# Kernel tuning notes

Hardware: AMD Instinct MI355X
Metric: run time of the kernel (lower is better)

## Reference

```python
import jax, jax.numpy as jnp
import numpy as np

D_MODEL = 1024
D_FF = 4096
N_EXPERTS = 8
TOP_K = 2
AUX_COEF = 0.01
ZLOSS_COEF = 0.001
EPS = 1e-9


def setup_inputs() -> dict:
    key = jax.random.key(0)
    k0, k1, k2, k3 = jax.random.split(key, 4)
    x = jax.random.normal(k0, (4, 2048, D_MODEL), dtype=jnp.float32)
    router_w = jax.random.normal(k1, (N_EXPERTS, D_MODEL), dtype=jnp.float32) * 0.02
    w1 = jax.random.normal(k2, (N_EXPERTS, D_FF, D_MODEL), dtype=jnp.float32) * 0.02
    b1 = jnp.zeros((N_EXPERTS, D_FF), dtype=jnp.float32)
    w2 = jax.random.normal(k3, (N_EXPERTS, D_MODEL, D_FF), dtype=jnp.float32) * 0.02
    b2 = jnp.zeros((N_EXPERTS, D_MODEL), dtype=jnp.float32)
    return {"x": x, "router_w": router_w, "w1": w1, "b1": b1, "w2": w2, "b2": b2}


def reference(x, router_w, w1, b1, w2, b2):
    B, T, D = x.shape
    N = B * T
    xf = x.reshape(N, D)

    # Router: logits [N, E], softmax probs, top-k selection + renormalized weights
    logits = jnp.einsum('nd,ed->ne', xf, router_w)
    probs = jax.nn.softmax(logits, axis=-1)
    topk_vals, topk_idx = jax.lax.top_k(probs, TOP_K)  # [N, K]
    topk_w = topk_vals / (topk_vals.sum(axis=-1, keepdims=True) + EPS)

    # Dense combine weights [N, E] (top-k indices are unique per row)
    combine = jnp.zeros((N, N_EXPERTS), dtype=xf.dtype)
    combine = combine.at[jnp.arange(N)[:, None], topk_idx].add(topk_w)

    # Per-expert MLP (fixed small loop over experts), weighted combine.
    # drop_tokens=False => no capacity truncation; masked-dense == gather/scatter math.
    y = jnp.zeros_like(xf)
    for e in range(N_EXPERTS):
        h = jax.nn.gelu(jnp.einsum('nd,fd->nf', xf, w1[e]) + b1[e], approximate=False)
        out_e = jnp.einsum('nf,df->nd', h, w2[e]) + b2[e]
        y = y + out_e * combine[:, e:e + 1]

    # Aux losses / stats
    importance = probs.sum(axis=0)                                   # [E]
    expert_load = jnp.zeros((N_EXPERTS,), jnp.float32).at[topk_idx.reshape(-1)].add(1.0)
    imp_n = importance / (importance.sum() + EPS)
    load_n = expert_load / (expert_load.sum() + EPS)
    balance_loss = N_EXPERTS * jnp.sum(imp_n * load_n)
    z_loss = jnp.mean(jax.nn.logsumexp(logits, axis=-1) ** 2)
    aux_loss = AUX_COEF * balance_loss + ZLOSS_COEF * z_loss

    return y.reshape(B, T, D), aux_loss, expert_load, importance
```

## Files before the change

### kernel.cpp

```cpp
#include <hip/hip_runtime.h>
#include <math.h>

#define NTOK 8192
#define DMODEL 1024
#define DFF 4096
#define NEXP 8
#define TILE 128
#define MAXTILES 136
#define MAXROWS (MAXTILES * TILE)
#define MOE_EPS 1e-9f
#define REG64 8192

typedef unsigned short u16;
typedef __bf16 bf16x8 __attribute__((ext_vector_type(8)));
typedef float f32x4 __attribute__((ext_vector_type(4)));

struct Ctrl {
    int counts[NEXP];
    int fill[NEXP];
    int padded_off[NEXP];
    int n_tiles;
    int tile_expert[MAXTILES];
    int tile_base[MAXTILES];
    int tile_valid[MAXTILES];
    float imp[NEXP];
    float zacc;
};

__device__ __forceinline__ u16 f2bf(float f) {
    unsigned u = __float_as_uint(f);
    unsigned r = u + 0x7fffu + ((u >> 16) & 1u);
    return (u16)(r >> 16);
}

__device__ __forceinline__ void load16(const void* g, void* l) {
    __builtin_amdgcn_global_load_lds((__attribute__((address_space(1))) void*)g,
                                     (__attribute__((address_space(3))) void*)l,
                                     16, 0, 0);
}

__device__ __forceinline__ float gelu_fast(float h) {
    float u = h * (1.5957691216f + 0.0713548162f * h * h);
    return h / (1.f + __expf(-u));
}

__global__ __launch_bounds__(256) void k_convert(const float* __restrict__ src,
                                                 u16* __restrict__ dst, int n4) {
    int i = blockIdx.x * 256 + threadIdx.x;
    int stride = gridDim.x * 256;
    for (; i < n4; i += stride) {
        float4 v = ((const float4*)src)[i];
        ushort4 o;
        o.x = f2bf(v.x); o.y = f2bf(v.y); o.z = f2bf(v.z); o.w = f2bf(v.w);
        ((ushort4*)dst)[i] = o;
    }
}

__global__ __launch_bounds__(256) void k_router(const float* __restrict__ x,
                                                const float* __restrict__ rw,
                                                u16* __restrict__ xb,
                                                int* __restrict__ top_idx,
                                                float* __restrict__ top_w,
                                                Ctrl* __restrict__ ctrl) {
    __shared__ float srw[NEXP * DMODEL];
    __shared__ float simp[NEXP];
    __shared__ float szl;
    int tid = threadIdx.x;
    for (int i = tid; i < NEXP * DMODEL / 4; i += 256)
        ((float4*)srw)[i] = ((const float4*)rw)[i];
    if (tid < NEXP) simp[tid] = 0.f;
    if (tid == 0) szl = 0.f;
    __syncthreads();

    int lane = tid & 63;
    int n = blockIdx.x * 4 + (tid >> 6);
    float p[NEXP];
#pragma unroll
    for (int e = 0; e < NEXP; ++e) p[e] = 0.f;
    const float4* xr = (const float4*)(x + (size_t)n * DMODEL);
    u16 xs[16];
#pragma unroll
    for (int j = 0; j < 4; ++j) {
        float4 xv = xr[lane * 4 + j];
        int d = (lane * 4 + j) * 4;
        xs[j * 4 + 0] = f2bf(xv.x);
        xs[j * 4 + 1] = f2bf(xv.y);
        xs[j * 4 + 2] = f2bf(xv.z);
        xs[j * 4 + 3] = f2bf(xv.w);
#pragma unroll
        for (int e = 0; e < NEXP; ++e) {
            const float* r = srw + e * DMODEL + d;
            p[e] += xv.x * r[0] + xv.y * r[1] + xv.z * r[2] + xv.w * r[3];
        }
    }
    {
        uint4* dst = (uint4*)(xb + (size_t)n * DMODEL + lane * 16);
        dst[0] = ((const uint4*)xs)[0];
        dst[1] = ((const uint4*)xs)[1];
    }
#pragma unroll
    for (int e = 0; e < NEXP; ++e) {
#pragma unroll
        for (int off = 32; off > 0; off >>= 1) p[e] += __shfl_xor(p[e], off);
    }
    if (lane == 0) {
        float m = p[0];
#pragma unroll
        for (int e = 1; e < NEXP; ++e) m = fmaxf(m, p[e]);
        float pr[NEXP];
        float s = 0.f;
#pragma unroll
        for (int e = 0; e < NEXP; ++e) { pr[e] = expf(p[e] - m); s += pr[e]; }
        float inv = 1.f / s;
#pragma unroll
        for (int e = 0; e < NEXP; ++e) pr[e] *= inv;
        float lse = m + logf(s);
        int i0 = 0; float v0 = pr[0];
#pragma unroll
        for (int e = 1; e < NEXP; ++e) if (pr[e] > v0) { v0 = pr[e]; i0 = e; }
        int i1 = -1; float v1 = -1.f;
#pragma unroll
        for (int e = 0; e < NEXP; ++e) if (e != i0 && pr[e] > v1) { v1 = pr[e]; i1 = e; }
        float den = v0 + v1 + MOE_EPS;
        top_idx[n * 2] = i0;
        top_idx[n * 2 + 1] = i1;
        top_w[n * 2] = v0 / den;
        top_w[n * 2 + 1] = v1 / den;
#pragma unroll
        for (int e = 0; e < NEXP; ++e) atomicAdd(&simp[e], pr[e]);
        atomicAdd(&szl, lse * lse);
    }
    __syncthreads();
    if (tid < NEXP) atomicAdd(&ctrl->imp[tid], simp[tid]);
    if (tid == 255) atomicAdd(&ctrl->zacc, szl);
}

__global__ __launch_bounds__(256) void k_build(const int* __restrict__ top_idx,
                                               Ctrl* __restrict__ ctrl,
                                               int* __restrict__ tok_idx,
                                               float* __restrict__ tok_w) {
    __shared__ int cnt[NEXP];
    __shared__ int off[NEXP];
    __shared__ int tiles[NEXP];
    int tid = threadIdx.x;
    if (tid < NEXP) cnt[tid] = 0;
    __syncthreads();
    for (int i = tid; i < NTOK * 2; i += 256) atomicAdd(&cnt[top_idx[i]], 1);
    __syncthreads();
    if (tid == 0) {
        int o = 0, t = 0;
        for (int e = 0; e < NEXP; ++e) {
            int c = cnt[e];
            int te = (c + TILE - 1) / TILE;
            ctrl->counts[e] = c;
            ctrl->padded_off[e] = o;
            off[e] = o;
            tiles[e] = te;
            for (int i = 0; i < te; ++i) {
                ctrl->tile_expert[t] = e;
                ctrl->tile_base[t] = o + i * TILE;
                int v = c - i * TILE;
                ctrl->tile_valid[t] = v > TILE ? TILE : v;
                ++t;
            }
            o += te * TILE;
        }
        ctrl->n_tiles = t;
    }
    __syncthreads();
    for (int e = 0; e < NEXP; ++e) {
        int start = off[e] + cnt[e];
        int end = off[e] + tiles[e] * TILE;
        for (int i = start + tid; i < end; i += 256) {
            tok_idx[i] = 0;
            tok_w[i] = 0.f;
        }
    }
}

__global__ __launch_bounds__(256) void k_fill(const int* __restrict__ top_idx,
                                              const float* __restrict__ top_w,
                                              Ctrl* __restrict__ ctrl,
                                              int* __restrict__ tok_idx,
                                              float* __restrict__ tok_w) {
    int n = blockIdx.x * 256 + threadIdx.x;
    if (n >= NTOK) return;
#pragma unroll
    for (int k = 0; k < 2; ++k) {
        int e = top_idx[n * 2 + k];
        int pos = atomicAdd(&ctrl->fill[e], 1);
        int slot = ctrl->padded_off[e] + pos;
        tok_idx[slot] = n;
        tok_w[slot] = top_w[n * 2 + k];
    }
}

#define KLOOPM97(STA, STB, NK)                                                        \
    for (int kt = 0; kt < (NK); ++kt) {                                               \
        STA(kt); STB(kt);                                                             \
        asm volatile("s_waitcnt vmcnt(0)" ::: "memory");                              \
        __builtin_amdgcn_s_barrier();                                                 \
        bf16x8 a[4], b[4];                                                            \
        _Pragma("unroll") for (int m = 0; m < 4; ++m) a[m] = *(const bf16x8*)(sA + aoff[m] + csw0); \
        _Pragma("unroll") for (int n = 0; n < 4; ++n) b[n] = *(const bf16x8*)(sB + boff[n] + csw0); \
        __builtin_amdgcn_s_setprio(1);                                                \
        _Pragma("unroll") for (int m = 0; m < 4; ++m)                                 \
            _Pragma("unroll") for (int n = 0; n < 4; ++n)                             \
                acc[m][n] = __builtin_amdgcn_mfma_f32_16x16x32_bf16(a[m], b[n], acc[m][n], 0, 0, 0); \
        __builtin_amdgcn_s_setprio(0);                                                \
        _Pragma("unroll") for (int m = 0; m < 4; ++m) a[m] = *(const bf16x8*)(sA + aoff[m] + csw1); \
        _Pragma("unroll") for (int n = 0; n < 4; ++n) b[n] = *(const bf16x8*)(sB + boff[n] + csw1); \
        __builtin_amdgcn_s_setprio(1);                                                \
        _Pragma("unroll") for (int m = 0; m < 4; ++m)                                 \
            _Pragma("unroll") for (int n = 0; n < 4; ++n)                             \
                acc[m][n] = __builtin_amdgcn_mfma_f32_16x16x32_bf16(a[m], b[n], acc[m][n], 0, 0, 0); \
        __builtin_amdgcn_s_setprio(0);                                                \
        __builtin_amdgcn_s_barrier();                                                 \
    }

__global__ __launch_bounds__(256, 4) void k_gemm1(const u16* __restrict__ xb,
                                                  const u16* __restrict__ w1b,
                                                  const float* __restrict__ b1,
                                                  const int* __restrict__ tok_idx,
                                                  const Ctrl* __restrict__ ctrl,
                                                  u16* __restrict__ H) {
    int flat = blockIdx.x;
    int t = (flat & 7) + ((flat >> 8) << 3);
    int n0 = ((flat >> 3) & 31) * TILE;
    if (t >= ctrl->n_tiles) return;
    int e = ctrl->tile_expert[t];
    int rbase = ctrl->tile_base[t];

    __shared__ __align__(16) u16 sA[REG64];
    __shared__ __align__(16) u16 sB[REG64];

    int tid = threadIdx.x;
    const u16* aS[4];
    const u16* bS[4];
    int fo[4];
#pragma unroll
    for (int q = 0; q < 4; ++q) {
        int f = q * 256 + tid;
        int row = f >> 3;
        int lc = (f & 7) ^ (row & 7);
        aS[q] = xb + (size_t)tok_idx[rbase + row] * DMODEL + lc * 8;
        bS[q] = w1b + (size_t)e * DFF * DMODEL + (size_t)(n0 + row) * DMODEL + lc * 8;
        fo[q] = f * 8;
    }

#define STA1(kt)                                                                      \
    do { _Pragma("unroll") for (int q = 0; q < 4; ++q)                                \
        load16(aS[q] + (kt) * 64, &sA[fo[q]]); } while (0)
#define STB1(kt)                                                                      \
    do { _Pragma("unroll") for (int q = 0; q < 4; ++q)                                \
        load16(bS[q] + (kt) * 64, &sB[fo[q]]); } while (0)

    int lane = tid & 63, w = tid >> 6;
    int wr = w >> 1, wc = w & 1;
    int l15 = lane & 15, lg = lane >> 4;
    int bank7 = l15 & 7;
    int csw0 = ((lg + 0) ^ bank7) * 8;
    int csw1 = ((lg + 4) ^ bank7) * 8;

    int aoff[4], boff[4];
#pragma unroll
    for (int m = 0; m < 4; ++m) aoff[m] = (wr * 64 + m * 16 + l15) * 64;
#pragma unroll
    for (int n = 0; n < 4; ++n) boff[n] = (wc * 64 + n * 16 + l15) * 64;

    f32x4 acc[4][4];
#pragma unroll
    for (int m = 0; m < 4; ++m)
#pragma unroll
        for (int n = 0; n < 4; ++n) acc[m][n] = (f32x4){0.f, 0.f, 0.f, 0.f};

    KLOOPM97(STA1, STB1, DMODEL / 64)
#undef STA1
#undef STB1

    float bias[4];
#pragma unroll
    for (int n = 0; n < 4; ++n) bias[n] = b1[e * DFF + n0 + wc * 64 + n * 16 + l15];
#pragma unroll
    for (int m = 0; m < 4; ++m)
#pragma unroll
        for (int n = 0; n < 4; ++n) {
            int gcol = n0 + wc * 64 + n * 16 + l15;
#pragma unroll
            for (int r = 0; r < 4; ++r) {
                int grow = wr * 64 + m * 16 + lg * 4 + r;
                float h = acc[m][n][r] + bias[n];
                H[(size_t)(rbase + grow) * DFF + gcol] = f2bf(gelu_fast(h));
            }
        }
}

__global__ __launch_bounds__(256, 4) void k_gemm2(const u16* __restrict__ H,
                                                  const u16* __restrict__ w2b,
                                                  const float* __restrict__ b2,
                                                  const int* __restrict__ tok_idx,
                                                  const float* __restrict__ tok_w,
                                                  const Ctrl* __restrict__ ctrl,
                                                  float* __restrict__ y) {
    int flat = blockIdx.x;
    int t = (flat & 7) + ((flat >> 6) << 3);
    int n0 = ((flat >> 3) & 7) * TILE;
    if (t >= ctrl->n_tiles) return;
    int e = ctrl->tile_expert[t];
    int rbase = ctrl->tile_base[t];
    int valid = ctrl->tile_valid[t];

    __shared__ __align__(16) u16 sA[REG64];
    __shared__ __align__(16) u16 sB[REG64];

    int tid = threadIdx.x;
    const u16* aS[4];
    const u16* bS[4];
    int fo[4];
#pragma unroll
    for (int q = 0; q < 4; ++q) {
        int f = q * 256 + tid;
        int row = f >> 3;
        int lc = (f & 7) ^ (row & 7);
        aS[q] = H + (size_t)(rbase + row) * DFF + lc * 8;
        bS[q] = w2b + (size_t)e * DMODEL * DFF + (size_t)(n0 + row) * DFF + lc * 8;
        fo[q] = f * 8;
    }

#define STA2(kt)                                                                      \
    do { _Pragma("unroll") for (int q = 0; q < 4; ++q)                                \
        load16(aS[q] + (kt) * 64, &sA[fo[q]]); } while (0)
#define STB2(kt)                                                                      \
    do { _Pragma("unroll") for (int q = 0; q < 4; ++q)                                \
        load16(bS[q] + (kt) * 64, &sB[fo[q]]); } while (0)

    int lane = tid & 63, w = tid >> 6;
    int wr = w >> 1, wc = w & 1;
    int l15 = lane & 15, lg = lane >> 4;
    int bank7 = l15 & 7;
    int csw0 = ((lg + 0) ^ bank7) * 8;
    int csw1 = ((lg + 4) ^ bank7) * 8;

    int aoff[4], boff[4];
#pragma unroll
    for (int m = 0; m < 4; ++m) aoff[m] = (wr * 64 + m * 16 + l15) * 64;
#pragma unroll
    for (int n = 0; n < 4; ++n) boff[n] = (wc * 64 + n * 16 + l15) * 64;

    f32x4 acc[4][4];
#pragma unroll
    for (int m = 0; m < 4; ++m)
#pragma unroll
        for (int n = 0; n < 4; ++n) acc[m][n] = (f32x4){0.f, 0.f, 0.f, 0.f};

    KLOOPM97(STA2, STB2, DFF / 64)
#undef STA2
#undef STB2

    float bias[4];
#pragma unroll
    for (int n = 0; n < 4; ++n) bias[n] = b2[e * DMODEL + n0 + wc * 64 + n * 16 + l15];
#pragma unroll
    for (int m = 0; m < 4; ++m)
#pragma unroll
        for (int n = 0; n < 4; ++n) {
            int gcol = n0 + wc * 64 + n * 16 + l15;
#pragma unroll
            for (int r = 0; r < 4; ++r) {
                int grow = wr * 64 + m * 16 + lg * 4 + r;
                if (grow < valid) {
                    int slot = rbase + grow;
                    int tok = tok_idx[slot];
                    float wgt = tok_w[slot];
                    unsafeAtomicAdd(&y[(size_t)tok * DMODEL + gcol],
                                    wgt * (acc[m][n][r] + bias[n]));
                }
            }
        }
}

__global__ void k_final(const Ctrl* __restrict__ ctrl, float* __restrict__ out) {
    if (blockIdx.x == 0 && threadIdx.x == 0) {
        float imp[NEXP], ld[NEXP];
        float imps = 0.f, loads = 0.f;
        for (int e = 0; e < NEXP; ++e) {
            imp[e] = ctrl->imp[e];
            ld[e] = (float)ctrl->counts[e];
            imps += imp[e];
            loads += ld[e];
        }
        float bal = 0.f;
        for (int e = 0; e < NEXP; ++e)
            bal += (imp[e] / (imps + MOE_EPS)) * (ld[e] / (loads + MOE_EPS));
        bal *= (float)NEXP;
        float z = ctrl->zacc / (float)NTOK;
        float aux = 0.01f * bal + 0.001f * z;
        size_t base = (size_t)NTOK * DMODEL;
        out[base] = aux;
        for (int e = 0; e < NEXP; ++e) out[base + 1 + e] = ld[e];
        for (int e = 0; e < NEXP; ++e) out[base + 9 + e] = imp[e];
    }
}

extern "C" void kernel_launch(void* const* d_in, const int* in_sizes, int n_in,
                              void* d_out, int out_size, void* d_ws, size_t ws_size,
                              hipStream_t stream) {
    (void)in_sizes; (void)n_in; (void)out_size; (void)ws_size;
    const float* x  = (const float*)d_in[0];
    const float* rw = (const float*)d_in[1];
    const float* w1 = (const float*)d_in[2];
    const float* b1 = (const float*)d_in[3];
    const float* w2 = (const float*)d_in[4];
    const float* b2 = (const float*)d_in[5];
    float* out = (float*)d_out;

    char* p = (char*)d_ws;
    Ctrl* ctrl = (Ctrl*)p;          p += 4096;
    u16* xb    = (u16*)p;           p += (size_t)NTOK * DMODEL * 2;
    u16* w1b   = (u16*)p;           p += (size_t)NEXP * DFF * DMODEL * 2;
    u16* w2b   = (u16*)p;           p += (size_t)NEXP * DMODEL * DFF * 2;
    u16* Hbuf  = (u16*)p;           p += (size_t)MAXROWS * DFF * 2;
    int* tok_idx = (int*)p;         p += (size_t)MAXROWS * 4;
    float* tok_w = (float*)p;       p += (size_t)MAXROWS * 4;
    int* tIdx  = (int*)p;           p += (size_t)NTOK * 2 * 4;
    float* tW  = (float*)p;         p += (size_t)NTOK * 2 * 4;

    hipMemsetAsync(ctrl, 0, sizeof(Ctrl), stream);
    hipMemsetAsync(d_out, 0, (size_t)NTOK * DMODEL * sizeof(float), stream);

    k_convert<<<2048, 256, 0, stream>>>(w1, w1b, NEXP * DFF * DMODEL / 4);
    k_convert<<<2048, 256, 0, stream>>>(w2, w2b, NEXP * DMODEL * DFF / 4);

    k_router<<<NTOK / 4, 256, 0, stream>>>(x, rw, xb, tIdx, tW, ctrl);
    k_build<<<1, 256, 0, stream>>>(tIdx, ctrl, tok_idx, tok_w);
    k_fill<<<NTOK / 256, 256, 0, stream>>>(tIdx, tW, ctrl, tok_idx, tok_w);

    k_gemm1<<<MAXTILES * (DFF / TILE), 256, 0, stream>>>(xb, w1b, b1, tok_idx, ctrl, Hbuf);
    k_gemm2<<<MAXTILES * (DMODEL / TILE), 256, 0, stream>>>(Hbuf, w2b, b2, tok_idx, tok_w, ctrl, out);

    k_final<<<1, 64, 0, stream>>>(ctrl, out);
}
```

Measured before the change: 694.5 us.

## Use persistent grids for expert GEMMs and merge small launches

Both expert GEMM kernels become persistent: a fixed grid of 1024 blocks strides over the tile work list, so blocks no longer launch only to exit on padded tiles. The two weight-conversion launches are merged into one kernel, and the aux-loss finalisation moves into k_build, which removes the k_final launch. The aim is lower launch and early-exit block overhead. The cost is a static striding over work, which can balance load worse than the hardware block scheduler, plus an extra barrier per tile.

After: 738.9 us. 6.4% more time.

```diff
diff --git a/kernel.cpp b/kernel.cpp
--- a/kernel.cpp
+++ b/kernel.cpp
@@ -10,6 +10,7 @@
 #define MAXROWS (MAXTILES * TILE)
 #define MOE_EPS 1e-9f
 #define REG64 8192
+#define PGRID 1024
 
 typedef unsigned short u16;
 typedef __bf16 bf16x8 __attribute__((ext_vector_type(8)));
@@ -44,15 +45,19 @@
     return h / (1.f + __expf(-u));
 }
 
-__global__ __launch_bounds__(256) void k_convert(const float* __restrict__ src,
-                                                 u16* __restrict__ dst, int n4) {
+__global__ __launch_bounds__(256) void k_convert2(const float* __restrict__ s1,
+                                                  u16* __restrict__ d1, int n4a,
+                                                  const float* __restrict__ s2,
+                                                  u16* __restrict__ d2, int n4tot) {
     int i = blockIdx.x * 256 + threadIdx.x;
     int stride = gridDim.x * 256;
-    for (; i < n4; i += stride) {
-        float4 v = ((const float4*)src)[i];
+    for (; i < n4tot; i += stride) {
+        const float4* src = (i < n4a) ? (const float4*)s1 + i : (const float4*)s2 + (i - n4a);
+        ushort4* dst = (i < n4a) ? (ushort4*)d1 + i : (ushort4*)d2 + (i - n4a);
+        float4 v = *src;
         ushort4 o;
         o.x = f2bf(v.x); o.y = f2bf(v.y); o.z = f2bf(v.z); o.w = f2bf(v.w);
-        ((ushort4*)dst)[i] = o;
+        *dst = o;
     }
 }
 
@@ -138,7 +143,8 @@
 __global__ __launch_bounds__(256) void k_build(const int* __restrict__ top_idx,
                                                Ctrl* __restrict__ ctrl,
                                                int* __restrict__ tok_idx,
-                                               float* __restrict__ tok_w) {
+                                               float* __restrict__ tok_w,
+                                               float* __restrict__ out) {
     __shared__ int cnt[NEXP];
     __shared__ int off[NEXP];
     __shared__ int tiles[NEXP];
@@ -166,6 +172,24 @@
             o += te * TILE;
         }
         ctrl->n_tiles = t;
+        float imp[NEXP], ld[NEXP];
+        float imps = 0.f, loads = 0.f;
+        for (int e = 0; e < NEXP; ++e) {
+            imp[e] = ctrl->imp[e];
+            ld[e] = (float)cnt[e];
+            imps += imp[e];
+            loads += ld[e];
+        }
+        float bal = 0.f;
+        for (int e = 0; e < NEXP; ++e)
+            bal += (imp[e] / (imps + MOE_EPS)) * (ld[e] / (loads + MOE_EPS));
+        bal *= (float)NEXP;
+        float z = ctrl->zacc / (float)NTOK;
+        float aux = 0.01f * bal + 0.001f * z;
+        size_t base = (size_t)NTOK * DMODEL;
+        out[base] = aux;
+        for (int e = 0; e < NEXP; ++e) out[base + 1 + e] = ld[e];
+        for (int e = 0; e < NEXP; ++e) out[base + 9 + e] = imp[e];
     }
     __syncthreads();
     for (int e = 0; e < NEXP; ++e) {
@@ -224,29 +248,43 @@
                                                   const int* __restrict__ tok_idx,
                                                   const Ctrl* __restrict__ ctrl,
                                                   u16* __restrict__ H) {
-    int flat = blockIdx.x;
-    int t = (flat & 7) + ((flat >> 8) << 3);
-    int n0 = ((flat >> 3) & 31) * TILE;
-    if (t >= ctrl->n_tiles) return;
-    int e = ctrl->tile_expert[t];
-    int rbase = ctrl->tile_base[t];
-
     __shared__ __align__(16) u16 sA[REG64];
     __shared__ __align__(16) u16 sB[REG64];
 
     int tid = threadIdx.x;
-    const u16* aS[4];
-    const u16* bS[4];
-    int fo[4];
-#pragma unroll
-    for (int q = 0; q < 4; ++q) {
-        int f = q * 256 + tid;
-        int row = f >> 3;
-        int lc = (f & 7) ^ (row & 7);
-        aS[q] = xb + (size_t)tok_idx[rbase + row] * DMODEL + lc * 8;
-        bS[q] = w1b + (size_t)e * DFF * DMODEL + (size_t)(n0 + row) * DMODEL + lc * 8;
-        fo[q] = f * 8;
-    }
+    int lane = tid & 63, w = tid >> 6;
+    int wr = w >> 1, wc = w & 1;
+    int l15 = lane & 15, lg = lane >> 4;
+    int bank7 = l15 & 7;
+    int csw0 = ((lg + 0) ^ bank7) * 8;
+    int csw1 = ((lg + 4) ^ bank7) * 8;
+
+    int aoff[4], boff[4];
+#pragma unroll
+    for (int m = 0; m < 4; ++m) aoff[m] = (wr * 64 + m * 16 + l15) * 64;
+#pragma unroll
+    for (int n = 0; n < 4; ++n) boff[n] = (wc * 64 + n * 16 + l15) * 64;
+
+    int n_tiles = ctrl->n_tiles;
+    for (int wk = blockIdx.x; wk < MAXTILES * 32; wk += PGRID) {
+        int t = (wk & 7) + ((wk >> 8) << 3);
+        int n0 = ((wk >> 3) & 31) * TILE;
+        if (t >= n_tiles) continue;
+        int e = ctrl->tile_expert[t];
+        int rbase = ctrl->tile_base[t];
+
+        const u16* aS[4];
+        const u16* bS[4];
+        int fo[4];
+#pragma unroll
+        for (int q = 0; q < 4; ++q) {
+            int f = q * 256 + tid;
+            int row = f >> 3;
+            int lc = (f & 7) ^ (row & 7);
+            aS[q] = xb + (size_t)tok_idx[rbase + row] * DMODEL + lc * 8;
+            bS[q] = w1b + (size_t)e * DFF * DMODEL + (size_t)(n0 + row) * DMODEL + lc * 8;
+            fo[q] = f * 8;
+        }
 
 #define STA1(kt)                                                                      \
     do { _Pragma("unroll") for (int q = 0; q < 4; ++q)                                \
@@ -255,44 +293,33 @@
     do { _Pragma("unroll") for (int q = 0; q < 4; ++q)                                \
         load16(bS[q] + (kt) * 64, &sB[fo[q]]); } while (0)
 
-    int lane = tid & 63, w = tid >> 6;
-    int wr = w >> 1, wc = w & 1;
-    int l15 = lane & 15, lg = lane >> 4;
-    int bank7 = l15 & 7;
-    int csw0 = ((lg + 0) ^ bank7) * 8;
-    int csw1 = ((lg + 4) ^ bank7) * 8;
-
-    int aoff[4], boff[4];
-#pragma unroll
-    for (int m = 0; m < 4; ++m) aoff[m] = (wr * 64 + m * 16 + l15) * 64;
-#pragma unroll
-    for (int n = 0; n < 4; ++n) boff[n] = (wc * 64 + n * 16 + l15) * 64;
-
-    f32x4 acc[4][4];
-#pragma unroll
-    for (int m = 0; m < 4; ++m)
-#pragma unroll
-        for (int n = 0; n < 4; ++n) acc[m][n] = (f32x4){0.f, 0.f, 0.f, 0.f};
-
-    KLOOPM97(STA1, STB1, DMODEL / 64)
+        f32x4 acc[4][4];
+#pragma unroll
+        for (int m = 0; m < 4; ++m)
+#pragma unroll
+            for (int n = 0; n < 4; ++n) acc[m][n] = (f32x4){0.f, 0.f, 0.f, 0.f};
+
+        KLOOPM97(STA1, STB1, DMODEL / 64)
 #undef STA1
 #undef STB1
 
-    float bias[4];
-#pragma unroll
-    for (int n = 0; n < 4; ++n) bias[n] = b1[e * DFF + n0 + wc * 64 + n * 16 + l15];
-#pragma unroll
-    for (int m = 0; m < 4; ++m)
-#pragma unroll
-        for (int n = 0; n < 4; ++n) {
-            int gcol = n0 + wc * 64 + n * 16 + l15;
-#pragma unroll
-            for (int r = 0; r < 4; ++r) {
-                int grow = wr * 64 + m * 16 + lg * 4 + r;
-                float h = acc[m][n][r] + bias[n];
-                H[(size_t)(rbase + grow) * DFF + gcol] = f2bf(gelu_fast(h));
+        float bias[4];
+#pragma unroll
+        for (int n = 0; n < 4; ++n) bias[n] = b1[e * DFF + n0 + wc * 64 + n * 16 + l15];
+#pragma unroll
+        for (int m = 0; m < 4; ++m)
+#pragma unroll
+            for (int n = 0; n < 4; ++n) {
+                int gcol = n0 + wc * 64 + n * 16 + l15;
+#pragma unroll
+                for (int r = 0; r < 4; ++r) {
+                    int grow = wr * 64 + m * 16 + lg * 4 + r;
+                    float h = acc[m][n][r] + bias[n];
+                    H[(size_t)(rbase + grow) * DFF + gcol] = f2bf(gelu_fast(h));
+                }
             }
-        }
+        __builtin_amdgcn_s_barrier();
+    }
 }
 
 __global__ __launch_bounds__(256, 4) void k_gemm2(const u16* __restrict__ H,
@@ -302,30 +329,44 @@
                                                   const float* __restrict__ tok_w,
                                                   const Ctrl* __restrict__ ctrl,
                                                   float* __restrict__ y) {
-    int flat = blockIdx.x;
-    int t = (flat & 7) + ((flat >> 6) << 3);
-    int n0 = ((flat >> 3) & 7) * TILE;
-    if (t >= ctrl->n_tiles) return;
-    int e = ctrl->tile_expert[t];
-    int rbase = ctrl->tile_base[t];
-    int valid = ctrl->tile_valid[t];
-
     __shared__ __align__(16) u16 sA[REG64];
     __shared__ __align__(16) u16 sB[REG64];
 
     int tid = threadIdx.x;
-    const u16* aS[4];
-    const u16* bS[4];
-    int fo[4];
-#pragma unroll
-    for (int q = 0; q < 4; ++q) {
-        int f = q * 256 + tid;
-        int row = f >> 3;
-        int lc = (f & 7) ^ (row & 7);
-        aS[q] = H + (size_t)(rbase + row) * DFF + lc * 8;
-        bS[q] = w2b + (size_t)e * DMODEL * DFF + (size_t)(n0 + row) * DFF + lc * 8;
-        fo[q] = f * 8;
-    }
+    int lane = tid & 63, w = tid >> 6;
+    int wr = w >> 1, wc = w & 1;
+    int l15 = lane & 15, lg = lane >> 4;
+    int bank7 = l15 & 7;
+    int csw0 = ((lg + 0) ^ bank7) * 8;
+    int csw1 = ((lg + 4) ^ bank7) * 8;
+
+    int aoff[4], boff[4];
+#pragma unroll
+    for (int m = 0; m < 4; ++m) aoff[m] = (wr * 64 + m * 16 + l15) * 64;
+#pragma unroll
+    for (int n = 0; n < 4; ++n) boff[n] = (wc * 64 + n * 16 + l15) * 64;
+
+    int n_tiles = ctrl->n_tiles;
+    for (int wk = blockIdx.x; wk < MAXTILES * 8; wk += PGRID) {
+        int t = (wk & 7) + ((wk >> 6) << 3);
+        int n0 = ((wk >> 3) & 7) * TILE;
+        if (t >= n_tiles) continue;
+        int e = ctrl->tile_expert[t];
+        int rbase = ctrl->tile_base[t];
+        int valid = ctrl->tile_valid[t];
+
+        const u16* aS[4];
+        const u16* bS[4];
+        int fo[4];
+#pragma unroll
+        for (int q = 0; q < 4; ++q) {
+            int f = q * 256 + tid;
+            int row = f >> 3;
+            int lc = (f & 7) ^ (row & 7);
+            aS[q] = H + (size_t)(rbase + row) * DFF + lc * 8;
+            bS[q] = w2b + (size_t)e * DMODEL * DFF + (size_t)(n0 + row) * DFF + lc * 8;
+            fo[q] = f * 8;
+        }
 
 #define STA2(kt)                                                                      \
     do { _Pragma("unroll") for (int q = 0; q < 4; ++q)                                \
@@ -334,71 +375,37 @@
     do { _Pragma("unroll") for (int q = 0; q < 4; ++q)                                \
         load16(bS[q] + (kt) * 64, &sB[fo[q]]); } while (0)
 
-    int lane = tid & 63, w = tid >> 6;
-    int wr = w >> 1, wc = w & 1;
-    int l15 = lane & 15, lg = lane >> 4;
-    int bank7 = l15 & 7;
-    int csw0 = ((lg + 0) ^ bank7) * 8;
-    int csw1 = ((lg + 4) ^ bank7) * 8;
-
-    int aoff[4], boff[4];
-#pragma unroll
-    for (int m = 0; m < 4; ++m) aoff[m] = (wr * 64 + m * 16 + l15) * 64;
-#pragma unroll
-    for (int n = 0; n < 4; ++n) boff[n] = (wc * 64 + n * 16 + l15) * 64;
-
-    f32x4 acc[4][4];
-#pragma unroll
-    for (int m = 0; m < 4; ++m)
-#pragma unroll
-        for (int n = 0; n < 4; ++n) acc[m][n] = (f32x4){0.f, 0.f, 0.f, 0.f};
-
-    KLOOPM97(STA2, STB2, DFF / 64)
+        f32x4 acc[4][4];
+#pragma unroll
+        for (int m = 0; m < 4; ++m)
+#pragma unroll
+            for (int n = 0; n < 4; ++n) acc[m][n] = (f32x4){0.f, 0.f, 0.f, 0.f};
+
+        KLOOPM97(STA2, STB2, DFF / 64)
 #undef STA2
 #undef STB2
 
-    float bias[4];
-#pragma unroll
-    for (int n = 0; n < 4; ++n) bias[n] = b2[e * DMODEL + n0 + wc * 64 + n * 16 + l15];
-#pragma unroll
-    for (int m = 0; m < 4; ++m)
-#pragma unroll
-        for (int n = 0; n < 4; ++n) {
-            int gcol = n0 + wc * 64 + n * 16 + l15;
-#pragma unroll
-            for (int r = 0; r < 4; ++r) {
-                int grow = wr * 64 + m * 16 + lg * 4 + r;
-                if (grow < valid) {
-                    int slot = rbase + grow;
-                    int tok = tok_idx[slot];
-                    float wgt = tok_w[slot];
-                    unsafeAtomicAdd(&y[(size_t)tok * DMODEL + gcol],
-                                    wgt * (acc[m][n][r] + bias[n]));
+        float bias[4];
+#pragma unroll
+        for (int n = 0; n < 4; ++n) bias[n] = b2[e * DMODEL + n0 + wc * 64 + n * 16 + l15];
+#pragma unroll
+        for (int m = 0; m < 4; ++m)
+#pragma unroll
+            for (int n = 0; n < 4; ++n) {
+                int gcol = n0 + wc * 64 + n * 16 + l15;
+#pragma unroll
+                for (int r = 0; r < 4; ++r) {
+                    int grow = wr * 64 + m * 16 + lg * 4 + r;
+                    if (grow < valid) {
+                        int slot = rbase + grow;
+                        int tok = tok_idx[slot];
+                        float wgt = tok_w[slot];
+                        unsafeAtomicAdd(&y[(size_t)tok * DMODEL + gcol],
+                                        wgt * (acc[m][n][r] + bias[n]));
+                    }
                 }
             }
-        }
-}
-
-__global__ void k_final(const Ctrl* __restrict__ ctrl, float* __restrict__ out) {
-    if (blockIdx.x == 0 && threadIdx.x == 0) {
-        float imp[NEXP], ld[NEXP];
-        float imps = 0.f, loads = 0.f;
-        for (int e = 0; e < NEXP; ++e) {
-            imp[e] = ctrl->imp[e];
-            ld[e] = (float)ctrl->counts[e];
-            imps += imp[e];
-            loads += ld[e];
-        }
-        float bal = 0.f;
-        for (int e = 0; e < NEXP; ++e)
-            bal += (imp[e] / (imps + MOE_EPS)) * (ld[e] / (loads + MOE_EPS));
-        bal *= (float)NEXP;
-        float z = ctrl->zacc / (float)NTOK;
-        float aux = 0.01f * bal + 0.001f * z;
-        size_t base = (size_t)NTOK * DMODEL;
-        out[base] = aux;
-        for (int e = 0; e < NEXP; ++e) out[base + 1 + e] = ld[e];
-        for (int e = 0; e < NEXP; ++e) out[base + 9 + e] = imp[e];
+        __builtin_amdgcn_s_barrier();
     }
 }
 
@@ -428,15 +435,13 @@
     hipMemsetAsync(ctrl, 0, sizeof(Ctrl), stream);
     hipMemsetAsync(d_out, 0, (size_t)NTOK * DMODEL * sizeof(float), stream);
 
-    k_convert<<<2048, 256, 0, stream>>>(w1, w1b, NEXP * DFF * DMODEL / 4);
-    k_convert<<<2048, 256, 0, stream>>>(w2, w2b, NEXP * DMODEL * DFF / 4);
+    int n4a = NEXP * DFF * DMODEL / 4;
+    k_convert2<<<2048, 256, 0, stream>>>(w1, w1b, n4a, w2, w2b, 2 * n4a);
 
     k_router<<<NTOK / 4, 256, 0, stream>>>(x, rw, xb, tIdx, tW, ctrl);
-    k_build<<<1, 256, 0, stream>>>(tIdx, ctrl, tok_idx, tok_w);
+    k_build<<<1, 256, 0, stream>>>(tIdx, ctrl, tok_idx, tok_w, out);
     k_fill<<<NTOK / 256, 256, 0, stream>>>(tIdx, tW, ctrl, tok_idx, tok_w);
 
-    k_gemm1<<<MAXTILES * (DFF / TILE), 256, 0, stream>>>(xb, w1b, b1, tok_idx, ctrl, Hbuf);
-    k_gemm2<<<MAXTILES * (DMODEL / TILE), 256, 0, stream>>>(Hbuf, w2b, b2, tok_idx, tok_w, ctrl, out);
-
-    k_final<<<1, 64, 0, stream>>>(ctrl, out);
-}
+    k_gemm1<<<PGRID, 256, 0, stream>>>(xb, w1b, b1, tok_idx, ctrl, Hbuf);
+    k_gemm2<<<PGRID, 256, 0, stream>>>(Hbuf, w2b, b2, tok_idx, tok_w, ctrl, out);
+}
```
